# Optimization experiments

Hardware: AMD Instinct MI355X
Metric: run time of the kernel (lower is better)

## Reference

```python
import jax, jax.numpy as jnp
import numpy as np

LN_EPS = 1e-6


def setup_inputs() -> dict:
    key = jax.random.key(0)
    ks = jax.random.split(key, 10)
    B, S, D, M, P = 64, 512, 1024, 512, 3
    seq_out = jax.random.normal(ks[0], (B, S, D), dtype=jnp.float32)
    # dependency-tree style adjacency: sparse 0/1, stored dense as in the module
    adj = (jax.random.uniform(ks[1], (B, S, S)) < 0.02).astype(jnp.float32)
    aspect_mask = jax.random.randint(ks[2], (B, S), 0, 2, dtype=jnp.int32)
    # guarantee at least one aspect token per row (asp_wn divisor)
    aspect_mask = aspect_mask.at[:, 0].set(1)
    sc = 0.02
    return {
        "seq_out": seq_out,
        "adj": adj,
        "aspect_mask": aspect_mask,
        "ln_a": jnp.ones((D,), jnp.float32),
        "ln_b": jnp.zeros((D,), jnp.float32),
        "asp_w": jax.random.normal(ks[3], (D,), jnp.float32) * sc,
        "asp_b": jnp.zeros((), jnp.float32),
        "W0": jax.random.normal(ks[4], (D, M), jnp.float32) * sc,
        "b0": jnp.zeros((M,), jnp.float32),
        "W1": jax.random.normal(ks[5], (M, M), jnp.float32) * sc,
        "b1": jnp.zeros((M,), jnp.float32),
        "W2": jax.random.normal(ks[6], (M, M), jnp.float32) * sc,
        "b2": jnp.zeros((M,), jnp.float32),
        "cls_w": jax.random.normal(ks[7], (2 * M, P), jnp.float32) * sc,
        "cls_b": jnp.zeros((P,), jnp.float32),
    }


def _torch_layernorm(x, a, b):
    # torch code: a*(x-mean)/(std+eps)+b with unbiased std (Bessel, /(D-1))
    D = x.shape[-1]
    mean = jnp.mean(x, axis=-1, keepdims=True)
    xc = x - mean
    std = jnp.sqrt(jnp.sum(xc * xc, axis=-1, keepdims=True) / (D - 1))
    return a * xc / (std + LN_EPS) + b


def reference(seq_out, adj, aspect_mask, ln_a, ln_b, asp_w, asp_b,
              W0, b0, W1, b1, W2, b2, cls_w, cls_b):
    tgt = aspect_mask.astype(seq_out.dtype)                 # [B,S] labels == BCE weight (eval mode)
    x = _torch_layernorm(seq_out, ln_a, ln_b)               # [B,S,D]

    # aspect classification head + weighted BCEWithLogits (mean over all elems)
    z = jnp.einsum('bsd,d->bs', x, asp_w) + asp_b           # logits [B,S]
    bce = jnp.logaddexp(0.0, z) - z * tgt                   # stable BCE-with-logits
    loss_asp = jnp.mean(tgt * bce)
    aspect_pred = jax.nn.sigmoid(z)

    # dense-adjacency GCN (dropout = identity in eval)
    denom = jnp.sum(adj, axis=2, keepdims=True) + 1.0       # [B,S,1]
    out = x
    for W, b in ((W0, b0), (W1, b1), (W2, b2)):
        Ax = jnp.einsum('bst,btd->bsd', adj, out)           # aggregate
        out = jax.nn.relu((Ax @ W + b) / denom)             # project + degree-norm + relu

    # aspect-masked mean pool + global mean pool
    asp_wn = jnp.sum(tgt, axis=1, keepdims=True)            # [B,1]
    dep = jnp.einsum('bsm,bs->bm', out, tgt) / asp_wn       # [B,M]
    glob = jnp.mean(out, axis=1)                            # [B,M]

    feature = jnp.concatenate([dep, glob], axis=-1) @ cls_w + cls_b
    logits = jax.nn.softmax(feature, axis=1)
    return feature, logits, aspect_pred, loss_asp
```

## Files before the change

### kernel.cpp

```cpp
#include <hip/hip_runtime.h>
#include <math.h>

typedef __bf16 bf16;
typedef bf16 bf16x2 __attribute__((ext_vector_type(2)));
typedef bf16 bf16x4 __attribute__((ext_vector_type(4)));
typedef bf16 bf16x8 __attribute__((ext_vector_type(8)));
typedef float f32x4 __attribute__((ext_vector_type(4)));

#define NROWS 32768
#define DDIM 1024
#define MDIM 512

__device__ __forceinline__ float wave_reduce_sum(float v) {
#pragma unroll
  for (int o = 32; o > 0; o >>= 1) v += __shfl_down(v, o, 64);
  return v;
}

__device__ __forceinline__ void load_lds16(const bf16* g, bf16* l) {
  __builtin_amdgcn_global_load_lds(
      (const __attribute__((address_space(1))) unsigned int*)g,
      (__attribute__((address_space(3))) unsigned int*)l, 16, 0, 0);
}

__global__ __launch_bounds__(256) void prep_kernel(
    const float* __restrict__ seq, const float* __restrict__ adj,
    const int* __restrict__ amask, const float* __restrict__ ga,
    const float* __restrict__ gb, const float* __restrict__ aw,
    const float* __restrict__ ab, const float* __restrict__ W0,
    const float* __restrict__ W1, const float* __restrict__ W2,
    bf16* __restrict__ xn, float* __restrict__ aspect_pred,
    float* __restrict__ loss_arr, unsigned short* __restrict__ nbr,
    int* __restrict__ cnt, float* __restrict__ denomv,
    bf16* __restrict__ W0T, bf16* __restrict__ W1T, bf16* __restrict__ W2T) {
  __shared__ float sh1[4], sh2[4], sh3[4];
  __shared__ int wcnt[4];
  const int bid = blockIdx.x;
  const int tid = threadIdx.x;

  if (bid < 32768) {
    const int row = bid;
    const float* xr = seq + (size_t)row * DDIM;
    float4 v = *(const float4*)&xr[tid * 4];
    float s = v.x + v.y + v.z + v.w;
    float sq = v.x * v.x + v.y * v.y + v.z * v.z + v.w * v.w;
    s = wave_reduce_sum(s);
    sq = wave_reduce_sum(sq);
    if ((tid & 63) == 0) { sh1[tid >> 6] = s; sh2[tid >> 6] = sq; }
    __syncthreads();
    s = sh1[0] + sh1[1] + sh1[2] + sh1[3];
    sq = sh2[0] + sh2[1] + sh2[2] + sh2[3];
    float mean = s * (1.0f / 1024.0f);
    float var = (sq - 1024.0f * mean * mean) * (1.0f / 1023.0f);
    var = fmaxf(var, 0.0f);
    float inv = 1.0f / (sqrtf(var) + 1e-6f);
    float4 a4 = *(const float4*)&ga[tid * 4];
    float4 b4 = *(const float4*)&gb[tid * 4];
    float4 w4 = *(const float4*)&aw[tid * 4];
    float x0 = a4.x * (v.x - mean) * inv + b4.x;
    float x1 = a4.y * (v.y - mean) * inv + b4.y;
    float x2 = a4.z * (v.z - mean) * inv + b4.z;
    float x3 = a4.w * (v.w - mean) * inv + b4.w;
    bf16x4 o;
    o[0] = (bf16)x0; o[1] = (bf16)x1; o[2] = (bf16)x2; o[3] = (bf16)x3;
    *(bf16x4*)&xn[(size_t)row * DDIM + tid * 4] = o;
    float zp = x0 * w4.x + x1 * w4.y + x2 * w4.z + x3 * w4.w;
    zp = wave_reduce_sum(zp);
    if ((tid & 63) == 0) sh3[tid >> 6] = zp;
    __syncthreads();
    if (tid == 0) {
      float z = sh3[0] + sh3[1] + sh3[2] + sh3[3] + ab[0];
      aspect_pred[row] = 1.0f / (1.0f + expf(-z));
      float tgt = (float)amask[row];
      float bce = fmaxf(z, 0.0f) + log1pf(expf(-fabsf(z))) - z * tgt;
      loss_arr[row] = tgt * bce;
    }
  } else if (bid < 65536) {
    const int row = bid - 32768;
    const int lane = tid & 63;
    const int wv = tid >> 6;
    const float* ar = adj + (size_t)row * 512;
    unsigned short* nr = nbr + (size_t)row * 512;
    float v0 = ar[wv * 128 + lane];
    float v1 = ar[wv * 128 + 64 + lane];
    unsigned long long m0 = __ballot(v0 != 0.0f);
    unsigned long long m1 = __ballot(v1 != 0.0f);
    int c0 = __popcll(m0), c1 = __popcll(m1);
    if (lane == 0) wcnt[wv] = c0 + c1;
    __syncthreads();
    int base = 0;
#pragma unroll
    for (int k = 0; k < 4; ++k) base += (k < wv) ? wcnt[k] : 0;
    unsigned long long below = (1ull << lane) - 1ull;
    if (v0 != 0.0f) nr[base + __popcll(m0 & below)] = (unsigned short)(wv * 128 + lane);
    if (v1 != 0.0f) nr[base + c0 + __popcll(m1 & below)] = (unsigned short)(wv * 128 + 64 + lane);
    if (tid == 0) {
      int tot = wcnt[0] + wcnt[1] + wcnt[2] + wcnt[3];
      cnt[row] = tot;
      denomv[row] = (float)tot + 1.0f;
    }
  } else {
    int e = (bid - 65536) * 256 + tid;
    if (e < 524288) {
      int n = e >> 10, k = e & 1023;
      W0T[e] = (bf16)W0[(size_t)k * 512 + n];
    } else if (e < 786432) {
      int e2 = e - 524288;
      int n = e2 >> 9, k = e2 & 511;
      W1T[e2] = (bf16)W1[(size_t)k * 512 + n];
    } else {
      int e3 = e - 786432;
      int n = e3 >> 9, k = e3 & 511;
      W2T[e3] = (bf16)W2[(size_t)k * 512 + n];
    }
  }
}

#define BAR  __builtin_amdgcn_s_barrier()
#define WAITL do { asm volatile("s_waitcnt lgkmcnt(0)" ::: "memory"); \
                   __builtin_amdgcn_sched_barrier(0); } while (0)
#define WAITV4 do { asm volatile("s_waitcnt vmcnt(4)" ::: "memory"); \
                    __builtin_amdgcn_sched_barrier(0); } while (0)

__global__ __launch_bounds__(512, 2) void gemm256(const bf16* __restrict__ A,
                                                  const bf16* __restrict__ BT,
                                                  bf16* __restrict__ C,
                                                  int K) {
  __shared__ __align__(16) bf16 SMEM[65536];
  bf16 (*As)[16384] = (bf16(*)[16384])SMEM;
  bf16 (*Bs)[16384] = (bf16(*)[16384])(SMEM + 32768);
  const int tid = threadIdx.x;
  const int lane = tid & 63;
  const int wave = tid >> 6;
  const int wr = wave >> 2;
  const int wc = wave & 3;
  const int T = K >> 6;

  const int p = blockIdx.x;
  const int chunk = gridDim.x >> 3;
  const int wg = (p & 7) * chunk + (p >> 3);
  const int m0 = (wg >> 1) * 256;
  const int n0 = (wg & 1) * 256;

  const int srow = tid >> 3;
  const int scol8 = (tid & 7) ^ (srow & 7);

#define STAGEA(t, h)                                                          \
  do {                                                                        \
    int kt_ = ((t) < T) ? (t) * 64 : 0;                                       \
    const bf16* s_ = A + (size_t)(m0 + (h) * 128 + srow) * K + kt_ + scol8*8; \
    bf16* d_ = &As[(t) & 1][(h) * 8192 + wave * 512];                         \
    load_lds16(s_, d_);                                                       \
    load_lds16(s_ + (size_t)64 * K, d_ + 4096);                               \
  } while (0)
#define STAGEB(t, h)                                                          \
  do {                                                                        \
    int kt_ = ((t) < T) ? (t) * 64 : 0;                                       \
    const bf16* s_ = BT + (size_t)(n0 + (h) * 128 + srow) * K + kt_ + scol8*8;\
    bf16* d_ = &Bs[(t) & 1][(h) * 8192 + wave * 512];                         \
    load_lds16(s_, d_);                                                       \
    load_lds16(s_ + (size_t)64 * K, d_ + 4096);                               \
  } while (0)

  const int abase = (wr * 128 + (lane & 15)) * 64 + (lane >> 4) * 8;
  const int bbase = (wc * 64 + (lane & 15)) * 64 + (lane >> 4) * 8;
  const int axor = (lane & 7) << 3;

  bf16x8 areg[4][2], breg[4][2];
  f32x4 acc[8][4];
#pragma unroll
  for (int i = 0; i < 8; ++i)
#pragma unroll
    for (int j = 0; j < 4; ++j)
#pragma unroll
      for (int r = 0; r < 4; ++r) acc[i][j][r] = 0.0f;

#define LDA(buf_, qm)                                                         \
  _Pragma("unroll") for (int i_ = 0; i_ < 4; ++i_)                            \
  _Pragma("unroll") for (int h2_ = 0; h2_ < 2; ++h2_)                         \
    areg[i_][h2_] = *(const bf16x8*)&As[buf_][                                \
        (abase + ((qm)*4 + i_) * 1024 + h2_ * 32) ^ axor];
#define LDB(buf_, qn)                                                         \
  _Pragma("unroll") for (int j_ = 0; j_ < 2; ++j_)                            \
  _Pragma("unroll") for (int h2_ = 0; h2_ < 2; ++h2_)                         \
    breg[(qn)*2 + j_][h2_] = *(const bf16x8*)&Bs[buf_][                       \
        (bbase + ((qn)*2 + j_) * 1024 + h2_ * 32) ^ axor];
#define MFMAQ(qm, qn)                                                         \
  __builtin_amdgcn_s_setprio(1);                                              \
  _Pragma("unroll") for (int i_ = 0; i_ < 4; ++i_)                            \
  _Pragma("unroll") for (int j_ = 0; j_ < 2; ++j_)                            \
  _Pragma("unroll") for (int h2_ = 0; h2_ < 2; ++h2_)                         \
    acc[(qm)*4 + i_][(qn)*2 + j_] = __builtin_amdgcn_mfma_f32_16x16x32_bf16(  \
        areg[i_][h2_], breg[(qn)*2 + j_][h2_], acc[(qm)*4 + i_][(qn)*2 + j_], \
        0, 0, 0);                                                             \
  __builtin_amdgcn_s_setprio(0);

  STAGEA(0, 0); STAGEA(0, 1); STAGEB(0, 0); STAGEB(0, 1);
  STAGEB(1, 0); STAGEB(1, 1);
  WAITV4;
  BAR;

  const int NIT = T >> 1;
  for (int it = 0; it < NIT; ++it) {
    const int t1 = 2 * it + 1, t2 = 2 * it + 2, t3 = 2 * it + 3;
    LDA(0, 0); LDB(0, 0); STAGEA(t1, 0);
    BAR; WAITL; MFMAQ(0, 0); BAR;
    LDB(0, 1); STAGEA(t1, 1);
    BAR; WAITL; MFMAQ(0, 1); BAR;
    LDA(0, 1); STAGEB(t2, 0);
    BAR; WAITL; MFMAQ(1, 0); BAR;
    STAGEB(t2, 1);
    BAR; WAITL; MFMAQ(1, 1); WAITV4; BAR;
    LDA(1, 0); LDB(1, 0); STAGEA(t2, 0);
    BAR; WAITL; MFMAQ(0, 0); BAR;
    LDB(1, 1); STAGEA(t2, 1);
    BAR; WAITL; MFMAQ(0, 1); BAR;
    LDA(1, 1); STAGEB(t3, 0);
    BAR; WAITL; MFMAQ(1, 0); BAR;
    STAGEB(t3, 1);
    BAR; WAITL; MFMAQ(1, 1); WAITV4; BAR;
  }

  const int cn = lane & 15;
  const int rb = (lane >> 4) * 4;
#pragma unroll
  for (int i = 0; i < 8; ++i)
#pragma unroll
    for (int j = 0; j < 4; ++j) {
      int row = wr * 128 + i * 16 + rb;
      int colb = wc * 64 + j * 16 + cn;
#pragma unroll
      for (int r = 0; r < 4; ++r)
        SMEM[((row + r) << 8) + (colb ^ (((row + r) & 7) << 4))] =
            (bf16)acc[i][j][r];
    }
  __syncthreads();
  const size_t cbase = (size_t)m0 * MDIM + n0;
#pragma unroll
  for (int q = 0; q < 16; ++q) {
    int e = q * 4096 + tid * 8;
    int row = e >> 8, col = e & 255;
    *(bf16x8*)&C[cbase + (size_t)row * MDIM + col] =
        *(const bf16x8*)&SMEM[(row << 8) + (col ^ ((row & 7) << 4))];
  }
}

__global__ __launch_bounds__(128) void agg_kernel(const bf16* __restrict__ P,
                                                  const unsigned short* __restrict__ nbr,
                                                  const int* __restrict__ cnt,
                                                  const float* __restrict__ denomv,
                                                  const float* __restrict__ bias,
                                                  bf16* __restrict__ outb) {
  int p = blockIdx.x;
  int row = (p & 7) * 4096 + (p >> 3);
  int tid = threadIdx.x;
  int b = row >> 9;
  __shared__ unsigned short nl[512];
  int n = cnt[row];
  for (int i = tid; i < n; i += 128) nl[i] = nbr[(size_t)row * 512 + i];
  __syncthreads();
  const bf16* Pb = P + ((size_t)(b << 9)) * MDIM;
  int col = tid * 4;
  float a0 = 0, a1 = 0, a2 = 0, a3 = 0;
  for (int e = 0; e < n; ++e) {
    bf16x4 v = *(const bf16x4*)&Pb[(size_t)nl[e] * MDIM + col];
    a0 += (float)v[0]; a1 += (float)v[1]; a2 += (float)v[2]; a3 += (float)v[3];
  }
  float inv = 1.0f / denomv[row];
  float4 bb = *(const float4*)&bias[col];
  bf16x4 o;
  o[0] = (bf16)fmaxf((a0 + bb.x) * inv, 0.0f);
  o[1] = (bf16)fmaxf((a1 + bb.y) * inv, 0.0f);
  o[2] = (bf16)fmaxf((a2 + bb.z) * inv, 0.0f);
  o[3] = (bf16)fmaxf((a3 + bb.w) * inv, 0.0f);
  *(bf16x4*)&outb[(size_t)row * MDIM + col] = o;
}

__global__ __launch_bounds__(512) void poolcls_kernel(
    const bf16* __restrict__ outb, const int* __restrict__ amask,
    const float* __restrict__ loss_arr, const float* __restrict__ cw,
    const float* __restrict__ cb, float* __restrict__ outp) {
  __shared__ float tg[512];
  __shared__ float featL[1024];
  __shared__ float shr[3][8];
  const int tid = threadIdx.x;
  const int b = blockIdx.x;

  if (b == 64) {
    float s = 0.0f;
    for (int i = tid; i < NROWS; i += 512) s += loss_arr[i];
    s = wave_reduce_sum(s);
    if ((tid & 63) == 0) shr[0][tid >> 6] = s;
    __syncthreads();
    if (tid == 0) {
      float t = 0.0f;
#pragma unroll
      for (int k = 0; k < 8; ++k) t += shr[0][k];
      outp[33152] = t * (1.0f / 32768.0f);
    }
    return;
  }

  tg[tid] = (float)amask[b * 512 + tid];
  __syncthreads();
  float wn = 0.0f;
#pragma unroll 8
  for (int s = 0; s < 512; ++s) wn += tg[s];
  float a = 0, t = 0;
  const bf16* ob = outb + (size_t)b * 512 * MDIM + tid;
  for (int s = 0; s < 512; ++s) {
    float v = (float)ob[(size_t)s * MDIM];
    a += v; t += v * tg[s];
  }
  featL[tid] = t / wn;
  featL[512 + tid] = a * (1.0f / 512.0f);
  __syncthreads();

  float f1 = featL[tid], f2 = featL[512 + tid];
  float p0 = f1 * cw[tid * 3 + 0] + f2 * cw[(512 + tid) * 3 + 0];
  float p1 = f1 * cw[tid * 3 + 1] + f2 * cw[(512 + tid) * 3 + 1];
  float p2 = f1 * cw[tid * 3 + 2] + f2 * cw[(512 + tid) * 3 + 2];
  p0 = wave_reduce_sum(p0);
  p1 = wave_reduce_sum(p1);
  p2 = wave_reduce_sum(p2);
  if ((tid & 63) == 0) {
    shr[0][tid >> 6] = p0; shr[1][tid >> 6] = p1; shr[2][tid >> 6] = p2;
  }
  __syncthreads();
  if (tid == 0) {
    float q0 = 0, q1 = 0, q2 = 0;
#pragma unroll
    for (int k = 0; k < 8; ++k) { q0 += shr[0][k]; q1 += shr[1][k]; q2 += shr[2][k]; }
    q0 += cb[0]; q1 += cb[1]; q2 += cb[2];
    outp[b * 3 + 0] = q0;
    outp[b * 3 + 1] = q1;
    outp[b * 3 + 2] = q2;
    float m = fmaxf(q0, fmaxf(q1, q2));
    float e0 = expf(q0 - m), e1 = expf(q1 - m), e2 = expf(q2 - m);
    float inv = 1.0f / (e0 + e1 + e2);
    outp[192 + b * 3 + 0] = e0 * inv;
    outp[192 + b * 3 + 1] = e1 * inv;
    outp[192 + b * 3 + 2] = e2 * inv;
  }
}

extern "C" void kernel_launch(void* const* d_in, const int* in_sizes, int n_in,
                              void* d_out, int out_size, void* d_ws, size_t ws_size,
                              hipStream_t stream) {
  const float* seq   = (const float*)d_in[0];
  const float* adj   = (const float*)d_in[1];
  const int*   amask = (const int*)d_in[2];
  const float* ln_a  = (const float*)d_in[3];
  const float* ln_b  = (const float*)d_in[4];
  const float* asp_w = (const float*)d_in[5];
  const float* asp_b = (const float*)d_in[6];
  const float* W0    = (const float*)d_in[7];
  const float* b0    = (const float*)d_in[8];
  const float* W1    = (const float*)d_in[9];
  const float* b1    = (const float*)d_in[10];
  const float* W2    = (const float*)d_in[11];
  const float* b2    = (const float*)d_in[12];
  const float* cls_w = (const float*)d_in[13];
  const float* cls_b = (const float*)d_in[14];
  float* out = (float*)d_out;

  char* w = (char*)d_ws;
  bf16* P             = (bf16*)w;           w += (size_t)NROWS * MDIM * 2;
  bf16* xn            = (bf16*)w;           w += (size_t)NROWS * DDIM * 2;
  bf16* outb          = (bf16*)w;           w += (size_t)NROWS * MDIM * 2;
  unsigned short* nbr = (unsigned short*)w; w += (size_t)NROWS * 512 * 2;
  int* cnt            = (int*)w;            w += (size_t)NROWS * 4;
  float* denomv       = (float*)w;          w += (size_t)NROWS * 4;
  float* loss_arr     = (float*)w;          w += (size_t)NROWS * 4;
  bf16* W0T           = (bf16*)w;           w += (size_t)512 * 1024 * 2;
  bf16* W1T           = (bf16*)w;           w += (size_t)512 * 512 * 2;
  bf16* W2T           = (bf16*)w;           w += (size_t)512 * 512 * 2;

  prep_kernel<<<69632, 256, 0, stream>>>(seq, adj, amask, ln_a, ln_b, asp_w,
                                         asp_b, W0, W1, W2, xn, out + 384,
                                         loss_arr, nbr, cnt, denomv, W0T, W1T,
                                         W2T);
  gemm256<<<256, 512, 0, stream>>>(xn, W0T, P, 1024);
  agg_kernel<<<NROWS, 128, 0, stream>>>(P, nbr, cnt, denomv, b0, outb);
  gemm256<<<256, 512, 0, stream>>>(outb, W1T, P, 512);
  agg_kernel<<<NROWS, 128, 0, stream>>>(P, nbr, cnt, denomv, b1, outb);
  gemm256<<<256, 512, 0, stream>>>(outb, W2T, P, 512);
  agg_kernel<<<NROWS, 128, 0, stream>>>(P, nbr, cnt, denomv, b2, outb);
  poolcls_kernel<<<65, 512, 0, stream>>>(outb, amask, loss_arr, cls_w, cls_b,
                                         out);
}
```

Measured before the change: 282.1 us.

## Use one wave per row in prep and split pooling into parallel partial sums

The LayerNorm and adjacency-compaction parts of the prep kernel now give each row to a single wave. Each lane handles 16 floats, so the reductions use shuffles only and the shared-memory barriers are gone. The weight transpose now reads float4 coalesced and writes scattered bf16. The pooling pass was previously 64 blocks walking 512 rows each; it becomes a 512-block partial-sum kernel followed by a small reduction in the classifier kernel. This adds one kernel launch and a partial-sum buffer in the workspace.

```diff
diff --git a/kernel.cpp b/kernel.cpp
--- a/kernel.cpp
+++ b/kernel.cpp
@@ -14,6 +14,11 @@
 __device__ __forceinline__ float wave_reduce_sum(float v) {
 #pragma unroll
   for (int o = 32; o > 0; o >>= 1) v += __shfl_down(v, o, 64);
+  return v;
+}
+__device__ __forceinline__ float wave_allreduce_sum(float v) {
+#pragma unroll
+  for (int o = 32; o > 0; o >>= 1) v += __shfl_xor(v, o, 64);
   return v;
 }
 
@@ -33,85 +38,99 @@
     float* __restrict__ loss_arr, unsigned short* __restrict__ nbr,
     int* __restrict__ cnt, float* __restrict__ denomv,
     bf16* __restrict__ W0T, bf16* __restrict__ W1T, bf16* __restrict__ W2T) {
-  __shared__ float sh1[4], sh2[4], sh3[4];
-  __shared__ int wcnt[4];
   const int bid = blockIdx.x;
   const int tid = threadIdx.x;
-
-  if (bid < 32768) {
-    const int row = bid;
+  const int lane = tid & 63;
+  const int wv = tid >> 6;
+
+  if (bid < 8192) {
+    const int row = bid * 4 + wv;
     const float* xr = seq + (size_t)row * DDIM;
-    float4 v = *(const float4*)&xr[tid * 4];
-    float s = v.x + v.y + v.z + v.w;
-    float sq = v.x * v.x + v.y * v.y + v.z * v.z + v.w * v.w;
-    s = wave_reduce_sum(s);
-    sq = wave_reduce_sum(sq);
-    if ((tid & 63) == 0) { sh1[tid >> 6] = s; sh2[tid >> 6] = sq; }
-    __syncthreads();
-    s = sh1[0] + sh1[1] + sh1[2] + sh1[3];
-    sq = sh2[0] + sh2[1] + sh2[2] + sh2[3];
+    float4 v[4];
+    float s = 0.0f, sq = 0.0f;
+#pragma unroll
+    for (int j = 0; j < 4; ++j) {
+      v[j] = *(const float4*)&xr[j * 256 + lane * 4];
+      s += v[j].x + v[j].y + v[j].z + v[j].w;
+      sq += v[j].x * v[j].x + v[j].y * v[j].y + v[j].z * v[j].z + v[j].w * v[j].w;
+    }
+    s = wave_allreduce_sum(s);
+    sq = wave_allreduce_sum(sq);
     float mean = s * (1.0f / 1024.0f);
     float var = (sq - 1024.0f * mean * mean) * (1.0f / 1023.0f);
     var = fmaxf(var, 0.0f);
     float inv = 1.0f / (sqrtf(var) + 1e-6f);
-    float4 a4 = *(const float4*)&ga[tid * 4];
-    float4 b4 = *(const float4*)&gb[tid * 4];
-    float4 w4 = *(const float4*)&aw[tid * 4];
-    float x0 = a4.x * (v.x - mean) * inv + b4.x;
-    float x1 = a4.y * (v.y - mean) * inv + b4.y;
-    float x2 = a4.z * (v.z - mean) * inv + b4.z;
-    float x3 = a4.w * (v.w - mean) * inv + b4.w;
-    bf16x4 o;
-    o[0] = (bf16)x0; o[1] = (bf16)x1; o[2] = (bf16)x2; o[3] = (bf16)x3;
-    *(bf16x4*)&xn[(size_t)row * DDIM + tid * 4] = o;
-    float zp = x0 * w4.x + x1 * w4.y + x2 * w4.z + x3 * w4.w;
+    float zp = 0.0f;
+#pragma unroll
+    for (int j = 0; j < 4; ++j) {
+      int c = j * 256 + lane * 4;
+      float4 a4 = *(const float4*)&ga[c];
+      float4 b4 = *(const float4*)&gb[c];
+      float4 w4 = *(const float4*)&aw[c];
+      float x0 = a4.x * (v[j].x - mean) * inv + b4.x;
+      float x1 = a4.y * (v[j].y - mean) * inv + b4.y;
+      float x2 = a4.z * (v[j].z - mean) * inv + b4.z;
+      float x3 = a4.w * (v[j].w - mean) * inv + b4.w;
+      bf16x4 o;
+      o[0] = (bf16)x0; o[1] = (bf16)x1; o[2] = (bf16)x2; o[3] = (bf16)x3;
+      *(bf16x4*)&xn[(size_t)row * DDIM + c] = o;
+      zp += x0 * w4.x + x1 * w4.y + x2 * w4.z + x3 * w4.w;
+    }
     zp = wave_reduce_sum(zp);
-    if ((tid & 63) == 0) sh3[tid >> 6] = zp;
-    __syncthreads();
-    if (tid == 0) {
-      float z = sh3[0] + sh3[1] + sh3[2] + sh3[3] + ab[0];
+    if (lane == 0) {
+      float z = zp + ab[0];
       aspect_pred[row] = 1.0f / (1.0f + expf(-z));
       float tgt = (float)amask[row];
       float bce = fmaxf(z, 0.0f) + log1pf(expf(-fabsf(z))) - z * tgt;
       loss_arr[row] = tgt * bce;
     }
-  } else if (bid < 65536) {
-    const int row = bid - 32768;
-    const int lane = tid & 63;
-    const int wv = tid >> 6;
+  } else if (bid < 16384) {
+    const int row = (bid - 8192) * 4 + wv;
     const float* ar = adj + (size_t)row * 512;
     unsigned short* nr = nbr + (size_t)row * 512;
-    float v0 = ar[wv * 128 + lane];
-    float v1 = ar[wv * 128 + 64 + lane];
-    unsigned long long m0 = __ballot(v0 != 0.0f);
-    unsigned long long m1 = __ballot(v1 != 0.0f);
-    int c0 = __popcll(m0), c1 = __popcll(m1);
-    if (lane == 0) wcnt[wv] = c0 + c1;
-    __syncthreads();
+    unsigned long long below = (1ull << lane) - 1ull;
     int base = 0;
 #pragma unroll
-    for (int k = 0; k < 4; ++k) base += (k < wv) ? wcnt[k] : 0;
-    unsigned long long below = (1ull << lane) - 1ull;
-    if (v0 != 0.0f) nr[base + __popcll(m0 & below)] = (unsigned short)(wv * 128 + lane);
-    if (v1 != 0.0f) nr[base + c0 + __popcll(m1 & below)] = (unsigned short)(wv * 128 + 64 + lane);
-    if (tid == 0) {
-      int tot = wcnt[0] + wcnt[1] + wcnt[2] + wcnt[3];
-      cnt[row] = tot;
-      denomv[row] = (float)tot + 1.0f;
-    }
+    for (int t = 0; t < 2; ++t) {
+      float4 v = *(const float4*)&ar[t * 256 + lane * 4];
+      unsigned long long m0 = __ballot(v.x != 0.0f);
+      unsigned long long m1 = __ballot(v.y != 0.0f);
+      unsigned long long m2 = __ballot(v.z != 0.0f);
+      unsigned long long m3 = __ballot(v.w != 0.0f);
+      int c0 = __popcll(m0), c1 = __popcll(m1), c2 = __popcll(m2);
+      int col = t * 256 + lane * 4;
+      if (v.x != 0.0f) nr[base + __popcll(m0 & below)] = (unsigned short)(col + 0);
+      if (v.y != 0.0f) nr[base + c0 + __popcll(m1 & below)] = (unsigned short)(col + 1);
+      if (v.z != 0.0f) nr[base + c0 + c1 + __popcll(m2 & below)] = (unsigned short)(col + 2);
+      if (v.w != 0.0f) nr[base + c0 + c1 + c2 + __popcll(m3 & below)] = (unsigned short)(col + 3);
+      base += c0 + c1 + c2 + __popcll(m3);
+    }
+    if (lane == 0) { cnt[row] = base; denomv[row] = (float)base + 1.0f; }
   } else {
-    int e = (bid - 65536) * 256 + tid;
+    int e = ((bid - 16384) * 256 + tid) * 4;
     if (e < 524288) {
-      int n = e >> 10, k = e & 1023;
-      W0T[e] = (bf16)W0[(size_t)k * 512 + n];
+      float4 v = *(const float4*)&W0[e];
+      int k = e >> 9, n = e & 511;
+      W0T[(size_t)(n + 0) * 1024 + k] = (bf16)v.x;
+      W0T[(size_t)(n + 1) * 1024 + k] = (bf16)v.y;
+      W0T[(size_t)(n + 2) * 1024 + k] = (bf16)v.z;
+      W0T[(size_t)(n + 3) * 1024 + k] = (bf16)v.w;
     } else if (e < 786432) {
       int e2 = e - 524288;
-      int n = e2 >> 9, k = e2 & 511;
-      W1T[e2] = (bf16)W1[(size_t)k * 512 + n];
+      float4 v = *(const float4*)&W1[e2];
+      int k = e2 >> 9, n = e2 & 511;
+      W1T[(size_t)(n + 0) * 512 + k] = (bf16)v.x;
+      W1T[(size_t)(n + 1) * 512 + k] = (bf16)v.y;
+      W1T[(size_t)(n + 2) * 512 + k] = (bf16)v.z;
+      W1T[(size_t)(n + 3) * 512 + k] = (bf16)v.w;
     } else {
       int e3 = e - 786432;
-      int n = e3 >> 9, k = e3 & 511;
-      W2T[e3] = (bf16)W2[(size_t)k * 512 + n];
+      float4 v = *(const float4*)&W2[e3];
+      int k = e3 >> 9, n = e3 & 511;
+      W2T[(size_t)(n + 0) * 512 + k] = (bf16)v.x;
+      W2T[(size_t)(n + 1) * 512 + k] = (bf16)v.y;
+      W2T[(size_t)(n + 2) * 512 + k] = (bf16)v.z;
+      W2T[(size_t)(n + 3) * 512 + k] = (bf16)v.w;
     }
   }
 }
@@ -276,12 +295,33 @@
   *(bf16x4*)&outb[(size_t)row * MDIM + col] = o;
 }
 
+__global__ __launch_bounds__(256) void pool_part(const bf16* __restrict__ outb,
+                                                 const int* __restrict__ amask,
+                                                 float* __restrict__ part) {
+  int b = blockIdx.x >> 3;
+  int slab = blockIdx.x & 7;
+  int tid = threadIdx.x;
+  int c0 = tid * 2;
+  const bf16* ob = outb + (size_t)(b * 512 + slab * 64) * MDIM + c0;
+  const int* am = amask + b * 512 + slab * 64;
+  float a0 = 0, a1 = 0, t0 = 0, t1 = 0;
+#pragma unroll 4
+  for (int s = 0; s < 64; ++s) {
+    bf16x2 v = *(const bf16x2*)&ob[(size_t)s * MDIM];
+    float tg = (float)am[s];
+    float v0 = (float)v[0], v1 = (float)v[1];
+    a0 += v0; a1 += v1; t0 += v0 * tg; t1 += v1 * tg;
+  }
+  float* pp = part + ((size_t)blockIdx.x) * 1024;
+  pp[c0] = t0; pp[c0 + 1] = t1;
+  pp[512 + c0] = a0; pp[512 + c0 + 1] = a1;
+}
+
 __global__ __launch_bounds__(512) void poolcls_kernel(
-    const bf16* __restrict__ outb, const int* __restrict__ amask,
+    const float* __restrict__ part, const int* __restrict__ amask,
     const float* __restrict__ loss_arr, const float* __restrict__ cw,
     const float* __restrict__ cb, float* __restrict__ outp) {
   __shared__ float tg[512];
-  __shared__ float featL[1024];
   __shared__ float shr[3][8];
   const int tid = threadIdx.x;
   const int b = blockIdx.x;
@@ -306,17 +346,16 @@
   float wn = 0.0f;
 #pragma unroll 8
   for (int s = 0; s < 512; ++s) wn += tg[s];
-  float a = 0, t = 0;
-  const bf16* ob = outb + (size_t)b * 512 * MDIM + tid;
-  for (int s = 0; s < 512; ++s) {
-    float v = (float)ob[(size_t)s * MDIM];
-    a += v; t += v * tg[s];
-  }
-  featL[tid] = t / wn;
-  featL[512 + tid] = a * (1.0f / 512.0f);
-  __syncthreads();
-
-  float f1 = featL[tid], f2 = featL[512 + tid];
+  float t = 0.0f, a = 0.0f;
+  const float* pp = part + (size_t)b * 8 * 1024;
+#pragma unroll
+  for (int k = 0; k < 8; ++k) {
+    t += pp[k * 1024 + tid];
+    a += pp[k * 1024 + 512 + tid];
+  }
+  float f1 = t / wn;
+  float f2 = a * (1.0f / 512.0f);
+
   float p0 = f1 * cw[tid * 3 + 0] + f2 * cw[(512 + tid) * 3 + 0];
   float p1 = f1 * cw[tid * 3 + 1] + f2 * cw[(512 + tid) * 3 + 1];
   float p2 = f1 * cw[tid * 3 + 2] + f2 * cw[(512 + tid) * 3 + 2];
@@ -372,11 +411,12 @@
   int* cnt            = (int*)w;            w += (size_t)NROWS * 4;
   float* denomv       = (float*)w;          w += (size_t)NROWS * 4;
   float* loss_arr     = (float*)w;          w += (size_t)NROWS * 4;
+  float* part         = (float*)w;          w += (size_t)512 * 1024 * 4;
   bf16* W0T           = (bf16*)w;           w += (size_t)512 * 1024 * 2;
   bf16* W1T           = (bf16*)w;           w += (size_t)512 * 512 * 2;
   bf16* W2T           = (bf16*)w;           w += (size_t)512 * 512 * 2;
 
-  prep_kernel<<<69632, 256, 0, stream>>>(seq, adj, amask, ln_a, ln_b, asp_w,
+  prep_kernel<<<17408, 256, 0, stream>>>(seq, adj, amask, ln_a, ln_b, asp_w,
                                          asp_b, W0, W1, W2, xn, out + 384,
                                          loss_arr, nbr, cnt, denomv, W0T, W1T,
                                          W2T);
@@ -386,6 +426,7 @@
   agg_kernel<<<NROWS, 128, 0, stream>>>(P, nbr, cnt, denomv, b1, outb);
   gemm256<<<256, 512, 0, stream>>>(outb, W2T, P, 512);
   agg_kernel<<<NROWS, 128, 0, stream>>>(P, nbr, cnt, denomv, b2, outb);
-  poolcls_kernel<<<65, 512, 0, stream>>>(outb, amask, loss_arr, cls_w, cls_b,
+  pool_part<<<512, 256, 0, stream>>>(outb, amask, part);
+  poolcls_kernel<<<65, 512, 0, stream>>>(part, amask, loss_arr, cls_w, cls_b,
                                          out);
 }
```

Result: faster. 266.0 us (-5.7%).
